# Optimization experiments

Hardware: AMD Instinct MI355X
Metric: run time of the kernel (lower is better)

Reference implementation:

```python
import jax, jax.numpy as jnp
import numpy as np

HAD_G = 32  # hadamard_group_size == MX block size (scales are [out, in//32])

# FP4 E2M1 magnitude grid and decision midpoints (round-to-nearest)
_FP4_LEVELS = jnp.array([0.0, 0.5, 1.0, 1.5, 2.0, 3.0, 4.0, 6.0], dtype=jnp.float32)
_FP4_MIDS = jnp.array([0.25, 0.75, 1.25, 1.75, 2.5, 3.5, 5.0], dtype=jnp.float32)


def _hadamard(n: int) -> np.ndarray:
    H = np.array([[1.0]], dtype=np.float32)
    while H.shape[0] < n:
        H = np.block([[H, H], [H, -H]])
    return H * (n ** -0.5)


def mxfp4_quant_dequant(v):
    """MXFP4 quantize-dequantize along the last axis (block of 32).
    v: [..., 32]. Shared power-of-2 scale per block (E8M0, absmax-based),
    elements rounded to nearest FP4 (E2M1) value. Straight-through estimator.
    """
    amax = jnp.max(jnp.abs(v), axis=-1, keepdims=True)
    # scale = 2^(floor(log2(amax)) - emax_fp4), emax_fp4 = 2 (6 = 1.5 * 2^2)
    e = jnp.floor(jnp.log2(jnp.maximum(amax, jnp.float32(1e-30)))) - 2.0
    scale = jnp.exp2(e)
    a = v / scale
    mag = jnp.minimum(jnp.abs(a), 6.0)
    q = _FP4_LEVELS[jnp.digitize(mag, _FP4_MIDS)] * jnp.sign(a)
    deq = q * scale
    # STE: identity gradient through the quantizer (matches custom autograd Fn)
    return v + jax.lax.stop_gradient(deq - v)


def _rotate_quant(t, H):
    """Per-group Hadamard rotation then MXFP4 quant-dequant. t: [N, K]."""
    N, K = t.shape
    tg = t.reshape(N, K // HAD_G, HAD_G)
    tr = jnp.einsum('ngh,hk->ngk', tg, H)  # rotate each 32-group
    return mxfp4_quant_dequant(tr).reshape(N, K)


def setup_inputs() -> dict:
    key = jax.random.key(0)
    kx, kw, kb = jax.random.split(key, 3)
    B, S, K, O = 4, 2048, 4096, 16384
    x = jax.random.normal(kx, (B, S, K), dtype=jnp.float32)
    weight = jax.random.normal(kw, (O, K), dtype=jnp.float32) * 0.02
    bias = jax.random.normal(kb, (O,), dtype=jnp.float32) * 0.01
    fwd_hadamard = jnp.asarray(_hadamard(HAD_G))
    return {"x": x, "weight": weight, "bias": bias, "fwd_hadamard": fwd_hadamard}


def reference(x, weight, bias, fwd_hadamard):
    B, S, K = x.shape
    O = weight.shape[0]
    xq = _rotate_quant(x.reshape(B * S, K), fwd_hadamard)   # deq(q(x H))
    wq = _rotate_quant(weight, fwd_hadamard)                # deq(q(W H))
    # H H^T = I, so (xH)(WH)^T approximates x W^T; GEMM runs on quantized values
    y = xq @ wq.T + bias
    return y.reshape(B, S, O)
```

## Files before the change

kernel.cpp:

```cpp
#include <hip/hip_runtime.h>

typedef unsigned short u16;
typedef unsigned int u32;
typedef unsigned char u8;
typedef int v8i __attribute__((ext_vector_type(8)));
typedef int v4i __attribute__((ext_vector_type(4)));
typedef float v16f __attribute__((ext_vector_type(16)));

#define INV_SQRT32 0.17677669529663688f

__global__ __launch_bounds__(256) void rotquant4_kernel(
    const float* __restrict__ T, u8* __restrict__ Q4, u8* __restrict__ S,
    int ngroups, int gpr , int ntk )
{
    int g = blockIdx.x * 256 + threadIdx.x;
    if (g >= ngroups) return;

    int row = g / gpr;
    int kb  = g - row * gpr;

    const float4* src = (const float4*)(T + (size_t)g * 32);
    float v[32];
#pragma unroll
    for (int i = 0; i < 8; ++i) {
        float4 t = src[i];
        v[i*4+0] = t.x; v[i*4+1] = t.y; v[i*4+2] = t.z; v[i*4+3] = t.w;
    }

#pragma unroll
    for (int s = 1; s < 32; s <<= 1) {
#pragma unroll
        for (int i = 0; i < 32; ++i) {
            if (!(i & s)) {
                float a = v[i], b = v[i | s];
                v[i] = a + b;
                v[i | s] = a - b;
            }
        }
    }

    float amax = 0.f;
#pragma unroll
    for (int i = 0; i < 32; ++i) {
        v[i] *= INV_SQRT32;
        amax = fmaxf(amax, fabsf(v[i]));
    }

    u32 ab = __float_as_uint(amax);
    int be = (int)(ab >> 23);
    u32 w[4] = {0u, 0u, 0u, 0u};
    u8 sbyte = 0;
    if (be >= 3) {
        sbyte = (u8)(be - 2);
        float iscale = __uint_as_float((u32)(256 - be) << 23);
#pragma unroll
        for (int i = 0; i < 32; ++i) {
            float a = v[i] * iscale;
            float m = fminf(fabsf(a), 6.0f);
            int c = (m < 0.25f) ? 0 :
                    (m < 0.75f) ? 1 :
                    (m < 1.25f) ? 2 :
                    (m < 1.75f) ? 3 :
                    (m < 2.5f)  ? 4 :
                    (m < 3.5f)  ? 5 :
                    (m < 5.0f)  ? 6 : 7;
            c |= (int)((__float_as_uint(a) >> 28) & 8u);
            w[i >> 3] |= (u32)c << (4 * (i & 7));
        }
    }

    size_t tile = (size_t)(row >> 7) * (size_t)ntk + (size_t)(kb >> 2);
    uint4 p; p.x = w[0]; p.y = w[1]; p.z = w[2]; p.w = w[3];
    *(uint4*)(Q4 + tile * 8192 + (size_t)(kb & 3) * 2048
              + (size_t)(row & 127) * 16) = p;
    S[tile * 512 + (size_t)(row & 127) * 4 + (kb & 3)] = sbyte;
}

__device__ __forceinline__ void gload16(const void* g, void* l)
{
    __builtin_amdgcn_global_load_lds(
        (__attribute__((address_space(1))) void*)g,
        (__attribute__((address_space(3))) void*)l, 16, 0, 0);
}

#define BUF_BYTES 26624

__global__ __launch_bounds__(256, 2) void gemm4_bias(
    const u8* __restrict__ A4, const u8* __restrict__ AS,
    const u8* __restrict__ B4, const u8* __restrict__ BS,
    const float* __restrict__ bias, float* __restrict__ C,
    int M, int N, int K)
{
    __shared__ __align__(16) u8 smem[2 * BUF_BYTES];

    const int tid  = threadIdx.x;
    const int wave = tid >> 6;
    const int lane = tid & 63;
    const int l31  = lane & 31;
    const int lhi  = lane >> 5;
    const int wm   = wave >> 1;
    const int wn   = wave & 1;
    const int ntk  = K >> 7;

    const int nbn = N >> 7;
    const int nbm = M >> 8;
    int nwg = gridDim.x;
    int bid = blockIdx.x;
    int bm, bn;
    if ((nwg & 7) == 0 && (nbm & 7) == 0) {
        int cpx = nwg >> 3;
        int c   = bid & 7;
        int r   = bid >> 3;
        int bpc = nbm >> 3;
        int lb  = __builtin_ctz(bpc);
        bm = c * bpc + (r & (bpc - 1));
        bn = r >> lb;
        (void)cpx;
    } else {
        bn = bid % nbn;
        bm = bid / nbn;
    }

    v16f acc[4][2];
#pragma unroll
    for (int i = 0; i < 4; ++i)
#pragma unroll
        for (int j = 0; j < 2; ++j)
#pragma unroll
            for (int r = 0; r < 16; ++r) acc[i][j][r] = 0.f;

    const size_t aTile0 = (size_t)(2 * bm + (wave >> 1)) * ntk;
    const int    aSub   = (wave & 1) * 4096;
    const size_t bTile0 = (size_t)bn * ntk;
    const size_t asTile = (size_t)(2 * bm + (lane >> 5)) * ntk;
    const int    asOfs  = (lane & 31) * 16 - lane * 16;
    const int    bsOfs  = (lane & 31) * 16 - lane * 16;

#define STAGE(bufofs, kt)                                                     \
    do {                                                                      \
        const u8* at_ = A4 + (aTile0 + (kt)) * 8192 + aSub + lane * 16;       \
        const u8* bt_ = B4 + (bTile0 + (kt)) * 8192 + wave * 2048 + lane * 16;\
        _Pragma("unroll")                                                     \
        for (int j = 0; j < 4; ++j)                                           \
            gload16(at_ + j * 1024,                                           \
                    smem + (bufofs) + wave * 4096 + j * 1024);                \
        _Pragma("unroll")                                                     \
        for (int j = 0; j < 2; ++j)                                           \
            gload16(bt_ + j * 1024,                                           \
                    smem + (bufofs) + 16384 + wave * 2048 + j * 1024);        \
        gload16(AS + (asTile + (kt)) * 512 + lane * 16 + asOfs,               \
                smem + (bufofs) + 24576);                                     \
        gload16(BS + (bTile0 + (kt)) * 512 + lane * 16 + bsOfs,               \
                smem + (bufofs) + 25600);                                     \
    } while (0)

#define COMPUTE(cofs)                                                         \
    do {                                                                      \
        u32 sa_[4], sb_[2];                                                   \
        _Pragma("unroll")                                                     \
        for (int mi = 0; mi < 4; ++mi)                                        \
            sa_[mi] = *(const u32*)(smem + (cofs) + 24576                     \
                                    + (wm * 128 + mi * 32 + l31) * 4);        \
        _Pragma("unroll")                                                     \
        for (int ni = 0; ni < 2; ++ni)                                        \
            sb_[ni] = *(const u32*)(smem + (cofs) + 25600                     \
                                    + (wn * 64 + ni * 32 + l31) * 4);        \
        _Pragma("unroll")                                                     \
        for (int ks = 0; ks < 2; ++ks) {                                      \
            const int s_  = ks * 2 + lhi;                                     \
            const int sh_ = s_ * 8;                                           \
            v8i af_[4], bf_[2];                                               \
            _Pragma("unroll")                                                 \
            for (int mi = 0; mi < 4; ++mi) {                                  \
                v4i t_ = *(const v4i*)(smem + (cofs) + wm * 8192 + s_ * 2048  \
                                       + (mi * 32 + l31) * 16);               \
                af_[mi] = __builtin_shufflevector(t_, t_, 0,1,2,3,-1,-1,-1,-1);\
            }                                                                 \
            _Pragma("unroll")                                                 \
            for (int ni = 0; ni < 2; ++ni) {                                  \
                v4i t_ = *(const v4i*)(smem + (cofs) + 16384 + s_ * 2048      \
                                       + (wn * 64 + ni * 32 + l31) * 16);     \
                bf_[ni] = __builtin_shufflevector(t_, t_, 0,1,2,3,-1,-1,-1,-1);\
            }                                                                 \
            _Pragma("unroll")                                                 \
            for (int mi = 0; mi < 4; ++mi) {                                  \
                int sA_ = (int)((sa_[mi] >> sh_) & 0xffu);                    \
                _Pragma("unroll")                                             \
                for (int ni = 0; ni < 2; ++ni) {                              \
                    int sB_ = (int)((sb_[ni] >> sh_) & 0xffu);                \
                    acc[mi][ni] = __builtin_amdgcn_mfma_scale_f32_32x32x64_f8f6f4(\
                        af_[mi], bf_[ni], acc[mi][ni], 4, 4, 0, sA_, 0, sB_); \
                }                                                             \
            }                                                                 \
        }                                                                     \
    } while (0)

    const int NT = K >> 7;

    STAGE(0, 0);
    for (int t = 0; t < NT - 1; ++t) {
        const int pofs = ((t + 1) & 1) * BUF_BYTES;
        STAGE(pofs, t + 1);
        asm volatile("s_waitcnt vmcnt(8)" ::: "memory");
        __builtin_amdgcn_s_barrier();
        asm volatile("" ::: "memory");
        COMPUTE((t & 1) * BUF_BYTES);
        __builtin_amdgcn_s_barrier();
        asm volatile("" ::: "memory");
    }
    asm volatile("s_waitcnt vmcnt(0)" ::: "memory");
    __builtin_amdgcn_s_barrier();
    asm volatile("" ::: "memory");
    COMPUTE(((NT - 1) & 1) * BUF_BYTES);

    const int cb = bn * 128 + wn * 64;
    const int rb = bm * 256 + wm * 128;
#pragma unroll
    for (int ni = 0; ni < 2; ++ni) {
        float bb = bias[cb + ni * 32 + l31];
#pragma unroll
        for (int mi = 0; mi < 4; ++mi) {
#pragma unroll
            for (int reg = 0; reg < 16; ++reg) {
                int row = (reg & 3) + 8 * (reg >> 2) + 4 * lhi;
                C[(size_t)(rb + mi * 32 + row) * N + cb + ni * 32 + l31]
                    = acc[mi][ni][reg] + bb;
            }
        }
    }
#undef STAGE
#undef COMPUTE
}

extern "C" void kernel_launch(void* const* d_in, const int* in_sizes, int n_in,
                              void* d_out, int out_size, void* d_ws, size_t ws_size,
                              hipStream_t stream)
{
    const float* x    = (const float*)d_in[0];
    const float* w    = (const float*)d_in[1];
    const float* bias = (const float*)d_in[2];

    const int O = in_sizes[2];
    const int K = in_sizes[1] / O;
    const int M = in_sizes[0] / K;

    u8* x4 = (u8*)d_ws;
    u8* w4 = x4 + (size_t)M * (K / 2);
    u8* xs = w4 + (size_t)O * (K / 2);
    u8* ws = xs + (size_t)M * (K / 32);

    const int gpr = K / 32;
    const int ntk = K / 128;
    const int gx = M * gpr;
    const int gw = O * gpr;
    rotquant4_kernel<<<(gx + 255) / 256, 256, 0, stream>>>(x, x4, xs, gx, gpr, ntk);
    rotquant4_kernel<<<(gw + 255) / 256, 256, 0, stream>>>(w, w4, ws, gw, gpr, ntk);

    dim3 grid((M / 256) * (O / 128));
    gemm4_bias<<<grid, 256, 0, stream>>>(x4, xs, w4, ws, bias, (float*)d_out,
                                         M, O, K);
}
```

Measured before the change: 493.0 us.

## Enlarge GEMM tile to 256x256 with 8 waves and triple-buffered phased pipeline

The MXFP4 GEMM now uses 512-thread workgroups computing 256x256 output tiles instead of 256x128, so each A tile is reused across twice as many columns. The k-loop becomes a three-buffer pipeline that prefetches two k-tiles ahead. Global-to-LDS loads are interleaved between four MFMA phases, each fenced by barriers with s_setprio raised during the MFMA work. The aim is to cut global traffic per FLOP and hide load latency, at the cost of more LDS (about 104 KB per block), many more barriers per iteration, and possibly lower occupancy.

```diff
diff --git a/kernel.cpp b/kernel.cpp
--- a/kernel.cpp
+++ b/kernel.cpp
@@ -82,40 +82,47 @@
         (__attribute__((address_space(1))) void*)g,
         (__attribute__((address_space(3))) void*)l, 16, 0, 0);
 }
-
-#define BUF_BYTES 26624
-
-__global__ __launch_bounds__(256, 2) void gemm4_bias(
+__device__ __forceinline__ void gload4(const void* g, void* l)
+{
+    __builtin_amdgcn_global_load_lds(
+        (__attribute__((address_space(1))) void*)g,
+        (__attribute__((address_space(3))) void*)l, 4, 0, 0);
+}
+
+#define BUF_BYTES 34816
+#define OFS_B     16384
+#define OFS_AS    32768
+#define OFS_BS    33792
+
+__global__ __launch_bounds__(512, 2) void gemm4_bias(
     const u8* __restrict__ A4, const u8* __restrict__ AS,
     const u8* __restrict__ B4, const u8* __restrict__ BS,
     const float* __restrict__ bias, float* __restrict__ C,
     int M, int N, int K)
 {
-    __shared__ __align__(16) u8 smem[2 * BUF_BYTES];
+    __shared__ __align__(16) u8 smem[3 * BUF_BYTES];
 
     const int tid  = threadIdx.x;
     const int wave = tid >> 6;
     const int lane = tid & 63;
     const int l31  = lane & 31;
     const int lhi  = lane >> 5;
-    const int wm   = wave >> 1;
-    const int wn   = wave & 1;
+    const int wm   = wave >> 2;
+    const int wn   = wave & 3;
     const int ntk  = K >> 7;
-
-    const int nbn = N >> 7;
+    const int NT   = ntk;
+
+    const int nbn = N >> 8;
     const int nbm = M >> 8;
-    int nwg = gridDim.x;
     int bid = blockIdx.x;
     int bm, bn;
-    if ((nwg & 7) == 0 && (nbm & 7) == 0) {
-        int cpx = nwg >> 3;
+    if (((gridDim.x & 7) == 0) && ((nbm & 7) == 0)) {
+        int bpc = nbm >> 3;
+        int lb  = __builtin_ctz(bpc);
         int c   = bid & 7;
         int r   = bid >> 3;
-        int bpc = nbm >> 3;
-        int lb  = __builtin_ctz(bpc);
         bm = c * bpc + (r & (bpc - 1));
         bn = r >> lb;
-        (void)cpx;
     } else {
         bn = bid % nbn;
         bm = bid / nbn;
@@ -129,91 +136,124 @@
 #pragma unroll
             for (int r = 0; r < 16; ++r) acc[i][j][r] = 0.f;
 
-    const size_t aTile0 = (size_t)(2 * bm + (wave >> 1)) * ntk;
-    const int    aSub   = (wave & 1) * 4096;
-    const size_t bTile0 = (size_t)bn * ntk;
-    const size_t asTile = (size_t)(2 * bm + (lane >> 5)) * ntk;
-    const int    asOfs  = (lane & 31) * 16 - lane * 16;
-    const int    bsOfs  = (lane & 31) * 16 - lane * 16;
-
-#define STAGE(bufofs, kt)                                                     \
-    do {                                                                      \
-        const u8* at_ = A4 + (aTile0 + (kt)) * 8192 + aSub + lane * 16;       \
-        const u8* bt_ = B4 + (bTile0 + (kt)) * 8192 + wave * 2048 + lane * 16;\
-        _Pragma("unroll")                                                     \
-        for (int j = 0; j < 4; ++j)                                           \
-            gload16(at_ + j * 1024,                                           \
-                    smem + (bufofs) + wave * 4096 + j * 1024);                \
-        _Pragma("unroll")                                                     \
-        for (int j = 0; j < 2; ++j)                                           \
-            gload16(bt_ + j * 1024,                                           \
-                    smem + (bufofs) + 16384 + wave * 2048 + j * 1024);        \
-        gload16(AS + (asTile + (kt)) * 512 + lane * 16 + asOfs,               \
-                smem + (bufofs) + 24576);                                     \
-        gload16(BS + (bTile0 + (kt)) * 512 + lane * 16 + bsOfs,               \
-                smem + (bufofs) + 25600);                                     \
-    } while (0)
-
-#define COMPUTE(cofs)                                                         \
-    do {                                                                      \
-        u32 sa_[4], sb_[2];                                                   \
-        _Pragma("unroll")                                                     \
-        for (int mi = 0; mi < 4; ++mi)                                        \
-            sa_[mi] = *(const u32*)(smem + (cofs) + 24576                     \
-                                    + (wm * 128 + mi * 32 + l31) * 4);        \
-        _Pragma("unroll")                                                     \
-        for (int ni = 0; ni < 2; ++ni)                                        \
-            sb_[ni] = *(const u32*)(smem + (cofs) + 25600                     \
-                                    + (wn * 64 + ni * 32 + l31) * 4);        \
-        _Pragma("unroll")                                                     \
-        for (int ks = 0; ks < 2; ++ks) {                                      \
-            const int s_  = ks * 2 + lhi;                                     \
-            const int sh_ = s_ * 8;                                           \
-            v8i af_[4], bf_[2];                                               \
-            _Pragma("unroll")                                                 \
-            for (int mi = 0; mi < 4; ++mi) {                                  \
-                v4i t_ = *(const v4i*)(smem + (cofs) + wm * 8192 + s_ * 2048  \
-                                       + (mi * 32 + l31) * 16);               \
-                af_[mi] = __builtin_shufflevector(t_, t_, 0,1,2,3,-1,-1,-1,-1);\
-            }                                                                 \
-            _Pragma("unroll")                                                 \
-            for (int ni = 0; ni < 2; ++ni) {                                  \
-                v4i t_ = *(const v4i*)(smem + (cofs) + 16384 + s_ * 2048      \
-                                       + (wn * 64 + ni * 32 + l31) * 16);     \
-                bf_[ni] = __builtin_shufflevector(t_, t_, 0,1,2,3,-1,-1,-1,-1);\
-            }                                                                 \
-            _Pragma("unroll")                                                 \
-            for (int mi = 0; mi < 4; ++mi) {                                  \
-                int sA_ = (int)((sa_[mi] >> sh_) & 0xffu);                    \
-                _Pragma("unroll")                                             \
-                for (int ni = 0; ni < 2; ++ni) {                              \
-                    int sB_ = (int)((sb_[ni] >> sh_) & 0xffu);                \
-                    acc[mi][ni] = __builtin_amdgcn_mfma_scale_f32_32x32x64_f8f6f4(\
-                        af_[mi], bf_[ni], acc[mi][ni], 4, 4, 0, sA_, 0, sB_); \
-                }                                                             \
-            }                                                                 \
-        }                                                                     \
-    } while (0)
-
-    const int NT = K >> 7;
-
-    STAGE(0, 0);
-    for (int t = 0; t < NT - 1; ++t) {
-        const int pofs = ((t + 1) & 1) * BUF_BYTES;
-        STAGE(pofs, t + 1);
-        asm volatile("s_waitcnt vmcnt(8)" ::: "memory");
+    const size_t aRow0 = (size_t)(2 * bm) * ntk;
+    const size_t bRow0 = (size_t)(2 * bn) * ntk;
+    const int isA = (wave < 4);
+    const int w4  = wave & 3;
+    const u8* scB = isA ? AS : BS;
+    const size_t scT = (size_t)((isA ? 2 * bm : 2 * bn) + (w4 >> 1)) * ntk;
+    const int scInner = (w4 & 1) * 256 + lane * 4;
+    const int scDst   = (isA ? OFS_AS : OFS_BS) + w4 * 256;
+    const int gOfs = wave * 1024 + lane * 16;
+    const int lOfs = wave * 1024;
+
+#define STG_A(bofs, kt, r)                                                    \
+    gload16(A4 + ((aRow0 + (size_t)(r) * ntk + (kt)) << 13) + gOfs,           \
+            smem + (bofs) + (r) * 8192 + lOfs)
+#define STG_B(bofs, kt, r)                                                    \
+    gload16(B4 + ((bRow0 + (size_t)(r) * ntk + (kt)) << 13) + gOfs,           \
+            smem + (bofs) + OFS_B + (r) * 8192 + lOfs)
+#define STG_S(bofs, kt)                                                       \
+    gload4(scB + ((scT + (kt)) << 9) + scInner, smem + (bofs) + scDst)
+
+#define RD_A(dst, mi, ks)                                                     \
+    do {                                                                      \
+        v4i t_ = *(const v4i*)(smem + cofs + wm * 8192                        \
+                               + ((ks) * 2 + lhi) * 2048                      \
+                               + ((mi) * 32 + l31) * 16);                     \
+        dst = __builtin_shufflevector(t_, t_, 0, 1, 2, 3, -1, -1, -1, -1);    \
+    } while (0)
+#define RD_B(dst, ni, ks)                                                     \
+    do {                                                                      \
+        v4i t_ = *(const v4i*)(smem + cofs + OFS_B + (wn >> 1) * 8192         \
+                               + ((ks) * 2 + lhi) * 2048                      \
+                               + (((wn & 1) * 64 + (ni) * 32 + l31)) * 16);   \
+        dst = __builtin_shufflevector(t_, t_, 0, 1, 2, 3, -1, -1, -1, -1);    \
+    } while (0)
+
+#define PH_SYNC()                                                             \
+    do {                                                                      \
+        __builtin_amdgcn_s_barrier();                                         \
+        asm volatile("s_waitcnt lgkmcnt(0)" ::: "memory");                    \
+        __builtin_amdgcn_sched_barrier(0);                                    \
+        __builtin_amdgcn_s_setprio(1);                                        \
+    } while (0)
+#define PH_END()                                                              \
+    do {                                                                      \
+        __builtin_amdgcn_s_setprio(0);                                        \
+        __builtin_amdgcn_s_barrier();                                         \
+    } while (0)
+
+#define MFMA4(aF0, aF1, miA, miB, ks)                                         \
+    do {                                                                      \
+        int sA0_ = (int)((saL[miA] >> ((ks) * 16)) & 0xffu);                  \
+        int sA1_ = (int)((saL[miB] >> ((ks) * 16)) & 0xffu);                  \
+        int sB0_ = (int)((sbL[0] >> ((ks) * 16)) & 0xffu);                    \
+        int sB1_ = (int)((sbL[1] >> ((ks) * 16)) & 0xffu);                    \
+        acc[miA][0] = __builtin_amdgcn_mfma_scale_f32_32x32x64_f8f6f4(        \
+            aF0, bf0, acc[miA][0], 4, 4, 0, sA0_, 0, sB0_);                   \
+        acc[miA][1] = __builtin_amdgcn_mfma_scale_f32_32x32x64_f8f6f4(        \
+            aF0, bf1, acc[miA][1], 4, 4, 0, sA0_, 0, sB1_);                   \
+        acc[miB][0] = __builtin_amdgcn_mfma_scale_f32_32x32x64_f8f6f4(        \
+            aF1, bf0, acc[miB][0], 4, 4, 0, sA1_, 0, sB0_);                   \
+        acc[miB][1] = __builtin_amdgcn_mfma_scale_f32_32x32x64_f8f6f4(        \
+            aF1, bf1, acc[miB][1], 4, 4, 0, sA1_, 0, sB1_);                   \
+    } while (0)
+
+    STG_A(0, 0, 0); STG_A(0, 0, 1); STG_B(0, 0, 0); STG_B(0, 0, 1); STG_S(0, 0);
+    STG_A(BUF_BYTES, 1, 0); STG_A(BUF_BYTES, 1, 1);
+    STG_B(BUF_BYTES, 1, 0); STG_B(BUF_BYTES, 1, 1); STG_S(BUF_BYTES, 1);
+    asm volatile("s_waitcnt vmcnt(5)" ::: "memory");
+    __builtin_amdgcn_s_barrier();
+
+    int cofs = 0;
+    int pofs = 2 * BUF_BYTES;
+    for (int t = 0; t < NT; ++t) {
+        const bool st = (t + 2 < NT);
+        const int kt2 = t + 2;
+        u32 saL[4], sbL[2];
+        v8i af0, af1, bf0, bf1;
+
+#pragma unroll
+        for (int mi = 0; mi < 4; ++mi)
+            saL[mi] = (*(const u32*)(smem + cofs + OFS_AS
+                                     + (wm * 128 + mi * 32 + l31) * 4)) >> (lhi * 8);
+#pragma unroll
+        for (int ni = 0; ni < 2; ++ni)
+            sbL[ni] = (*(const u32*)(smem + cofs + OFS_BS
+                                     + (wn * 64 + ni * 32 + l31) * 4)) >> (lhi * 8);
+        RD_A(af0, 0, 0); RD_A(af1, 1, 0); RD_B(bf0, 0, 0); RD_B(bf1, 1, 0);
+        if (st) { STG_A(pofs, kt2, 0); STG_A(pofs, kt2, 1); }
+        PH_SYNC();
+        MFMA4(af0, af1, 0, 1, 0);
+        PH_END();
+
+        RD_A(af0, 2, 0); RD_A(af1, 3, 0);
+        if (st) STG_B(pofs, kt2, 0);
+        PH_SYNC();
+        MFMA4(af0, af1, 2, 3, 0);
+        PH_END();
+
+        RD_A(af0, 0, 1); RD_A(af1, 1, 1); RD_B(bf0, 0, 1); RD_B(bf1, 1, 1);
+        if (st) STG_B(pofs, kt2, 1);
+        PH_SYNC();
+        MFMA4(af0, af1, 0, 1, 1);
+        PH_END();
+
+        RD_A(af0, 2, 1); RD_A(af1, 3, 1);
+        if (st) STG_S(pofs, kt2);
+        PH_SYNC();
+        MFMA4(af0, af1, 2, 3, 1);
+        __builtin_amdgcn_s_setprio(0);
+        if (st) asm volatile("s_waitcnt vmcnt(5)" ::: "memory");
+        else    asm volatile("s_waitcnt vmcnt(0)" ::: "memory");
         __builtin_amdgcn_s_barrier();
-        asm volatile("" ::: "memory");
-        COMPUTE((t & 1) * BUF_BYTES);
-        __builtin_amdgcn_s_barrier();
-        asm volatile("" ::: "memory");
-    }
-    asm volatile("s_waitcnt vmcnt(0)" ::: "memory");
-    __builtin_amdgcn_s_barrier();
-    asm volatile("" ::: "memory");
-    COMPUTE(((NT - 1) & 1) * BUF_BYTES);
-
-    const int cb = bn * 128 + wn * 64;
+
+        cofs += BUF_BYTES; if (cofs == 3 * BUF_BYTES) cofs = 0;
+        pofs += BUF_BYTES; if (pofs == 3 * BUF_BYTES) pofs = 0;
+    }
+
+    const int cb = bn * 256 + wn * 64;
     const int rb = bm * 256 + wm * 128;
 #pragma unroll
     for (int ni = 0; ni < 2; ++ni) {
@@ -228,8 +268,14 @@
             }
         }
     }
-#undef STAGE
-#undef COMPUTE
+#undef STG_A
+#undef STG_B
+#undef STG_S
+#undef RD_A
+#undef RD_B
+#undef PH_SYNC
+#undef PH_END
+#undef MFMA4
 }
 
 extern "C" void kernel_launch(void* const* d_in, const int* in_sizes, int n_in,
@@ -256,7 +302,7 @@
     rotquant4_kernel<<<(gx + 255) / 256, 256, 0, stream>>>(x, x4, xs, gx, gpr, ntk);
     rotquant4_kernel<<<(gw + 255) / 256, 256, 0, stream>>>(w, w4, ws, gw, gpr, ntk);
 
-    dim3 grid((M / 256) * (O / 128));
-    gemm4_bias<<<grid, 256, 0, stream>>>(x4, xs, w4, ws, bias, (float*)d_out,
+    dim3 grid((M / 256) * (O / 256));
+    gemm4_bias<<<grid, 512, 0, stream>>>(x4, xs, w4, ws, bias, (float*)d_out,
                                          M, O, K);
 }
```

Measured after the change: 508.7 us. 3.2% more time.
